# Kernel tuning notes

Hardware: AMD Instinct MI355X
Metric: run time of the kernel (lower is better)

Reference implementation:

```python
import jax, jax.numpy as jnp
import numpy as np

B, S, D, H = 2, 2048, 1024, 16
DK = D // H


def setup_inputs() -> dict:
    key = jax.random.key(0)
    ks = jax.random.split(key, 12)
    scale = 1.0 / np.sqrt(D)
    inp = {
        "Q": jax.random.normal(ks[0], (B, S, D), jnp.float32),
        "K": jax.random.normal(ks[1], (B, S, D), jnp.float32),
        "V": jax.random.normal(ks[2], (B, S, D), jnp.float32),
        # causal mask, broadcastable to [B, H, S, S]; 0 -> masked
        "Mask": jnp.tril(jnp.ones((S, S), jnp.int32))[None, None],
        "Wq": jax.random.normal(ks[3], (D, D), jnp.float32) * scale,
        "bq": jnp.zeros((D,), jnp.float32),
        "Wk": jax.random.normal(ks[4], (D, D), jnp.float32) * scale,
        "bk": jnp.zeros((D,), jnp.float32),
        "Wv": jax.random.normal(ks[5], (D, D), jnp.float32) * scale,
        "bv": jnp.zeros((D,), jnp.float32),
        "Wo": jax.random.normal(ks[6], (D, D), jnp.float32) * scale,
        "bo": jnp.zeros((D,), jnp.float32),
    }
    return inp


def _heads(x):
    # [B, S, D] -> [B, H, S, DK]
    return x.reshape(B, S, H, DK).transpose(0, 2, 1, 3)


def reference(Q, K, V, Mask, Wq, bq, Wk, bk, Wv, bv, Wo, bo):
    q = _heads(Q @ Wq.T + bq)
    k = _heads(K @ Wk.T + bk)
    v = _heads(V @ Wv.T + bv)
    # NOTE: original module does NOT scale by 1/sqrt(d_k)
    logits = jnp.einsum("bhqd,bhkd->bhqk", q, k)
    logits = jnp.where(Mask == 0, jnp.float32(-1e9), logits)
    attn = jax.nn.softmax(logits, axis=-1)  # dropout p=0.0 -> identity
    ctx = jnp.einsum("bhqk,bhkd->bhqd", attn, v)
    ctx = ctx.transpose(0, 2, 1, 3).reshape(B, S, D)
    return ctx @ Wo.T + bo
```

## Files before the change

### kernel.cpp

```cpp
#include <hip/hip_runtime.h>
#include <hip/hip_bf16.h>

#define B_  2
#define S_  2048
#define D_  1024
#define H_  16
#define DK_ 64
#define M_  (B_ * S_)

typedef __bf16 bf16;
typedef __bf16 bf16x8 __attribute__((ext_vector_type(8)));
typedef __bf16 bf16x4 __attribute__((ext_vector_type(4)));
typedef float  f32x4  __attribute__((ext_vector_type(4)));

#define MFMA16(a, b, c) __builtin_amdgcn_mfma_f32_16x16x32_bf16((a), (b), (c), 0, 0, 0)

__device__ __forceinline__ void gl2lds16(const bf16* g, bf16* l) {
    __builtin_amdgcn_global_load_lds((const __attribute__((address_space(1))) void*)g,
                                     (__attribute__((address_space(3))) void*)l, 16, 0, 0);
}

struct CastArgs { const float* src[7]; bf16* dst[7]; };

__global__ __launch_bounds__(256) void cast_all(CastArgs a) {
    int i = blockIdx.x * 256 + threadIdx.x;
    int seg, off;
    if (i < 3145728) { seg = i >> 20; off = i & 1048575; }
    else { int j = i - 3145728; seg = 3 + (j >> 18); off = j & 262143; }
    float4 v = ((const float4*)a.src[seg])[off];
    bf16x4 o;
    o[0] = (bf16)v.x; o[1] = (bf16)v.y; o[2] = (bf16)v.z; o[3] = (bf16)v.w;
    *(bf16x4*)&a.dst[seg][(size_t)off * 4] = o;
}

struct QkvArgs { const bf16* A[3]; const bf16* W[3]; const float* bias[3]; bf16* out[3]; };

__global__ __launch_bounds__(256, 3) void gemm_qkv(QkvArgs ar) {
    __shared__ char smem[34816];
    bf16* As = (bf16*)smem;
    bf16* Bs = (bf16*)(smem + 16384);
    bf16* Cs = (bf16*)smem;

    const int hid = (blockIdx.z * gridDim.y + blockIdx.y) * gridDim.x + blockIdx.x;
    const int swz = (hid & 7) * 96 + (hid >> 3);
    const int bx = swz & 7, by = (swz >> 3) & 31, z = swz >> 8;

    const bf16* A  = ar.A[z];
    const bf16* Bt = ar.W[z];
    const float* bias = ar.bias[z];
    bf16* Out = ar.out[z];
    const int mode = (z == 2) ? 1 : 0;

    const int t = threadIdx.x, lane = t & 63, w = t >> 6;
    const int lr = lane & 15, lq = lane >> 4;
    const int wm = (w >> 1) * 64, wn = (w & 1) * 64;
    const int n0 = bx * 128, m0 = by * 128;

    const bf16* Ag[4]; const bf16* Bg[4]; bf16* Al[4]; bf16* Bl[4];
#pragma unroll
    for (int i = 0; i < 4; ++i) {
        int c = i * 256 + w * 64 + lane;
        int row = c >> 3, x = (c & 7) ^ (row & 7);
        Ag[i] = A  + (size_t)(m0 + row) * 1024 + x * 8;
        Bg[i] = Bt + (size_t)(n0 + row) * 1024 + x * 8;
        Al[i] = As + (i * 256 + w * 64) * 8;
        Bl[i] = Bs + (i * 256 + w * 64) * 8;
    }

    f32x4 acc[4][4];
#pragma unroll
    for (int mi = 0; mi < 4; ++mi)
#pragma unroll
        for (int ni = 0; ni < 4; ++ni) acc[mi][ni] = 0.0f;

    for (int k0 = 0; k0 < 1024; k0 += 64) {
        __syncthreads();
#pragma unroll
        for (int i = 0; i < 4; ++i) {
            gl2lds16(Ag[i] + k0, Al[i]);
            gl2lds16(Bg[i] + k0, Bl[i]);
        }
        __syncthreads();
#pragma unroll
        for (int ks = 0; ks < 2; ++ks) {
            bf16x8 af[4], bfr[4];
#pragma unroll
            for (int mi = 0; mi < 4; ++mi) {
                int row = wm + mi * 16 + lr;
                af[mi] = *(const bf16x8*)&As[row * 64 + ((ks * 4 + lq) ^ (row & 7)) * 8];
            }
#pragma unroll
            for (int ni = 0; ni < 4; ++ni) {
                int row = wn + ni * 16 + lr;
                bfr[ni] = *(const bf16x8*)&Bs[row * 64 + ((ks * 4 + lq) ^ (row & 7)) * 8];
            }
#pragma unroll
            for (int mi = 0; mi < 4; ++mi)
#pragma unroll
                for (int ni = 0; ni < 4; ++ni) acc[mi][ni] = MFMA16(af[mi], bfr[ni], acc[mi][ni]);
        }
    }

    if (mode == 0) {
#pragma unroll
        for (int mi = 0; mi < 4; ++mi) {
#pragma unroll
            for (int ni = 0; ni < 4; ++ni) {
                int gn = n0 + wn + ni * 16 + lr;
                float bv = bias[gn];
#pragma unroll
                for (int r = 0; r < 4; ++r) {
                    int gm = m0 + wm + mi * 16 + lq * 4 + r;
                    float v = acc[mi][ni][r] + bv;
                    int b = gm >> 11, s = gm & (S_ - 1);
                    int h = gn >> 6, dk = gn & 63;
                    Out[(((size_t)(b * H_ + h) * S_ + s) << 6) + dk] = (bf16)v;
                }
            }
        }
    } else {
        __syncthreads();
#pragma unroll
        for (int mi = 0; mi < 4; ++mi) {
#pragma unroll
            for (int ni = 0; ni < 4; ++ni) {
                int n = wn + ni * 16 + lr;
                float bv = bias[n0 + n];
                bf16x4 pk;
#pragma unroll
                for (int r = 0; r < 4; ++r) pk[r] = (bf16)(acc[mi][ni][r] + bv);
                *(bf16x4*)&Cs[n * 136 + wm + mi * 16 + lq * 4] = pk;
            }
        }
        __syncthreads();
        const int b = m0 >> 11, s0 = m0 & (S_ - 1);
#pragma unroll
        for (int j = 0; j < 8; ++j) {
            int cc = j * 256 + t;
            int n = cc >> 4, cm = cc & 15;
            int gn = n0 + n, h = gn >> 6, dk = gn & 63;
            bf16x8 v = *(const bf16x8*)&Cs[n * 136 + cm * 8];
            *(bf16x8*)&Out[(((size_t)(b * H_ + h) * DK_ + dk) << 11) + s0 + cm * 8] = v;
        }
    }
}

__global__ __launch_bounds__(256, 2) void gemm_out(const bf16* __restrict__ A,
                                                   const bf16* __restrict__ Bt,
                                                   const float* __restrict__ bias,
                                                   float* __restrict__ Out) {
    __shared__ bf16 As[64 * 64];
    __shared__ bf16 Bs[128 * 64];

    const int hid = blockIdx.y * gridDim.x + blockIdx.x;
    const int swz = (hid & 7) * 64 + (hid >> 3);
    const int bx = swz & 7, by = swz >> 3;

    const int t = threadIdx.x, lane = t & 63, w = t >> 6;
    const int lr = lane & 15, lq = lane >> 4;
    const int wm = (w >> 1) * 32, wn = (w & 1) * 64;
    const int n0 = bx * 128, m0 = by * 64;

    const bf16* Ag[2]; bf16* Al[2];
#pragma unroll
    for (int i = 0; i < 2; ++i) {
        int c = i * 256 + w * 64 + lane;
        int row = c >> 3, x = (c & 7) ^ (row & 7);
        Ag[i] = A + (size_t)(m0 + row) * 1024 + x * 8;
        Al[i] = As + (i * 256 + w * 64) * 8;
    }
    const bf16* Bg[4]; bf16* Bl[4];
#pragma unroll
    for (int i = 0; i < 4; ++i) {
        int c = i * 256 + w * 64 + lane;
        int row = c >> 3, x = (c & 7) ^ (row & 7);
        Bg[i] = Bt + (size_t)(n0 + row) * 1024 + x * 8;
        Bl[i] = Bs + (i * 256 + w * 64) * 8;
    }

    f32x4 acc[2][4];
#pragma unroll
    for (int mi = 0; mi < 2; ++mi)
#pragma unroll
        for (int ni = 0; ni < 4; ++ni) acc[mi][ni] = 0.0f;

    for (int k0 = 0; k0 < 1024; k0 += 64) {
        __syncthreads();
#pragma unroll
        for (int i = 0; i < 2; ++i) gl2lds16(Ag[i] + k0, Al[i]);
#pragma unroll
        for (int i = 0; i < 4; ++i) gl2lds16(Bg[i] + k0, Bl[i]);
        __syncthreads();
#pragma unroll
        for (int ks = 0; ks < 2; ++ks) {
            bf16x8 af[2], bfr[4];
#pragma unroll
            for (int mi = 0; mi < 2; ++mi) {
                int row = wm + mi * 16 + lr;
                af[mi] = *(const bf16x8*)&As[row * 64 + ((ks * 4 + lq) ^ (row & 7)) * 8];
            }
#pragma unroll
            for (int ni = 0; ni < 4; ++ni) {
                int row = wn + ni * 16 + lr;
                bfr[ni] = *(const bf16x8*)&Bs[row * 64 + ((ks * 4 + lq) ^ (row & 7)) * 8];
            }
#pragma unroll
            for (int mi = 0; mi < 2; ++mi)
#pragma unroll
                for (int ni = 0; ni < 4; ++ni) acc[mi][ni] = MFMA16(af[mi], bfr[ni], acc[mi][ni]);
        }
    }

#pragma unroll
    for (int mi = 0; mi < 2; ++mi) {
#pragma unroll
        for (int ni = 0; ni < 4; ++ni) {
            int gn = n0 + wn + ni * 16 + lr;
            float bv = bias[gn];
#pragma unroll
            for (int r = 0; r < 4; ++r) {
                int gm = m0 + wm + mi * 16 + lq * 4 + r;
                Out[(size_t)gm * 1024 + gn] = acc[mi][ni][r] + bv;
            }
        }
    }
}

__global__ __launch_bounds__(256, 2) void flash_attn(const bf16* __restrict__ qh,
                                                     const bf16* __restrict__ kh,
                                                     const bf16* __restrict__ vt,
                                                     bf16* __restrict__ ctx) {
    __shared__ char smem[33280];
    bf16* Ks = (bf16*)smem;
    bf16* Ps = (bf16*)(smem + 16384);
    float* Op = (float*)(smem + 16384);
    float* Lh = (float*)(smem + 32768);

    const int id = blockIdx.x;
    const int xcd = id & 7, loc = id >> 3;
    const int bh = xcd * 4 + (loc & 3);
    const int pair = loc >> 2;
    const int b = bh >> 4, h = bh & 15;

    const bf16* Qp = qh + (size_t)bh * S_ * DK_;
    const bf16* Kp = kh + (size_t)bh * S_ * DK_;
    const bf16* Vp = vt + (size_t)bh * DK_ * S_;

    const int t = threadIdx.x, lane = t & 63, w = t >> 6;
    const int lr = lane & 15, lq = lane >> 4;
    const int wq = w & 1, wk = w >> 1;
    bf16* Pw = Ps + w * 2048;

    for (int half = 0; half < 2; ++half) {
        const int qt = half ? (31 - pair) : pair;

        bf16x8 qreg[2][2];
#pragma unroll
        for (int ks = 0; ks < 2; ++ks)
#pragma unroll
            for (int nt = 0; nt < 2; ++nt)
                qreg[ks][nt] = *(const bf16x8*)(Qp +
                    (size_t)(qt * 64 + wq * 32 + nt * 16 + lr) * 64 + ks * 32 + lq * 8);

        f32x4 oacc[2][4];
#pragma unroll
        for (int mt = 0; mt < 2; ++mt)
#pragma unroll
            for (int nt = 0; nt < 4; ++nt) oacc[mt][nt] = 0.0f;
        float lpart[2] = {0.f, 0.f};

        const int nkt = qt / 2 + 1;
        for (int kt = 0; kt < nkt; ++kt) {
            __syncthreads();
#pragma unroll
            for (int i = 0; i < 4; ++i) {
                int c = w * 256 + i * 64 + lane;
                int krow = c >> 3, xx = (c & 7) ^ (krow & 7);
                gl2lds16(Kp + (size_t)(kt * 128 + krow) * 64 + xx * 8, Ks + (w * 256 + i * 64) * 8);
            }
            __syncthreads();

            const int k64 = kt * 2 + wk;
            if (k64 <= qt) {
                bf16x8 bv[2][4];
#pragma unroll
                for (int kk = 0; kk < 2; ++kk)
#pragma unroll
                    for (int nt = 0; nt < 4; ++nt)
                        bv[kk][nt] = *(const bf16x8*)(Vp + (size_t)(nt * 16 + lr) * S_ +
                                                      kt * 128 + wk * 64 + kk * 32 + lq * 8);
                f32x4 s[4][2];
#pragma unroll
                for (int mt = 0; mt < 4; ++mt)
#pragma unroll
                    for (int nt = 0; nt < 2; ++nt) s[mt][nt] = 0.0f;
                __builtin_amdgcn_s_setprio(1);
#pragma unroll
                for (int ks = 0; ks < 2; ++ks) {
                    bf16x8 af[4];
                    int xx = (ks * 4 + lq) ^ (lr & 7);
#pragma unroll
                    for (int mt = 0; mt < 4; ++mt)
                        af[mt] = *(const bf16x8*)&Ks[(wk * 64 + mt * 16 + lr) * 64 + xx * 8];
#pragma unroll
                    for (int mt = 0; mt < 4; ++mt)
#pragma unroll
                        for (int nt = 0; nt < 2; ++nt) s[mt][nt] = MFMA16(af[mt], qreg[ks][nt], s[mt][nt]);
                }
                __builtin_amdgcn_s_setprio(0);
                const bool diag = (k64 == qt);
#pragma unroll
                for (int mt = 0; mt < 4; ++mt)
#pragma unroll
                    for (int nt = 0; nt < 2; ++nt) {
                        bf16x4 pb;
#pragma unroll
                        for (int r = 0; r < 4; ++r) {
                            int kl = mt * 16 + lq * 4 + r;
                            int qlT = wq * 32 + nt * 16 + lr;
                            float p = (!diag || kl <= qlT) ? __expf(s[mt][nt][r]) : 0.0f;
                            bf16 p16 = (bf16)p;
                            lpart[nt] += (float)p16;
                            pb[r] = p16;
                        }
                        int xx = (2 * mt + (lq >> 1)) ^ (lr & 7);
                        *(bf16x4*)&Pw[(nt * 16 + lr) * 64 + xx * 8 + (lq & 1) * 4] = pb;
                    }
                __builtin_amdgcn_s_setprio(1);
#pragma unroll
                for (int kk = 0; kk < 2; ++kk) {
                    bf16x8 ap[2];
                    int xx = (kk * 4 + lq) ^ (lr & 7);
#pragma unroll
                    for (int mt2 = 0; mt2 < 2; ++mt2)
                        ap[mt2] = *(const bf16x8*)&Pw[(mt2 * 16 + lr) * 64 + xx * 8];
#pragma unroll
                    for (int mt2 = 0; mt2 < 2; ++mt2)
#pragma unroll
                        for (int nt = 0; nt < 4; ++nt)
                            oacc[mt2][nt] = MFMA16(ap[mt2], bv[kk][nt], oacc[mt2][nt]);
                }
                __builtin_amdgcn_s_setprio(0);
            }
        }

        __syncthreads();
#pragma unroll
        for (int nt = 0; nt < 2; ++nt) {
            lpart[nt] += __shfl_xor(lpart[nt], 16);
            lpart[nt] += __shfl_xor(lpart[nt], 32);
        }
        if (lq == 0)
#pragma unroll
            for (int nt = 0; nt < 2; ++nt) Lh[wk * 64 + wq * 32 + nt * 16 + lr] = lpart[nt];
        if (wk == 1) {
#pragma unroll
            for (int mt = 0; mt < 2; ++mt)
#pragma unroll
                for (int nt = 0; nt < 4; ++nt)
#pragma unroll
                    for (int r = 0; r < 4; ++r) {
                        int row = mt * 16 + lq * 4 + r, col = nt * 16 + lr;
                        int xx = (col >> 2) ^ (row & 15);
                        Op[wq * 2048 + row * 64 + xx * 4 + (col & 3)] = oacc[mt][nt][r];
                    }
        }
        __syncthreads();
        if (wk == 0) {
            float linv[2][4];
#pragma unroll
            for (int mt = 0; mt < 2; ++mt)
#pragma unroll
                for (int r = 0; r < 4; ++r) {
                    int qq = wq * 32 + mt * 16 + lq * 4 + r;
                    linv[mt][r] = 1.0f / (Lh[qq] + Lh[64 + qq]);
                }
#pragma unroll
            for (int mt = 0; mt < 2; ++mt)
#pragma unroll
                for (int nt = 0; nt < 4; ++nt)
#pragma unroll
                    for (int r = 0; r < 4; ++r) {
                        int row = mt * 16 + lq * 4 + r, col = nt * 16 + lr;
                        int xx = (col >> 2) ^ (row & 15);
                        float v = (oacc[mt][nt][r] + Op[wq * 2048 + row * 64 + xx * 4 + (col & 3)]) * linv[mt][r];
                        int q = qt * 64 + wq * 32 + row;
                        ctx[((size_t)(b * S_ + q)) * D_ + h * DK_ + col] = (bf16)v;
                    }
        }
        __syncthreads();
    }
}

extern "C" void kernel_launch(void* const* d_in, const int* in_sizes, int n_in,
                              void* d_out, int out_size, void* d_ws, size_t ws_size,
                              hipStream_t stream) {
    const float* Q  = (const float*)d_in[0];
    const float* K  = (const float*)d_in[1];
    const float* V  = (const float*)d_in[2];
    const float* Wq = (const float*)d_in[4];
    const float* bq = (const float*)d_in[5];
    const float* Wk = (const float*)d_in[6];
    const float* bk = (const float*)d_in[7];
    const float* Wv = (const float*)d_in[8];
    const float* bv = (const float*)d_in[9];
    const float* Wo = (const float*)d_in[10];
    const float* bo = (const float*)d_in[11];

    char* p = (char*)d_ws;
    bf16* Qb  = (bf16*)p;  p += (size_t)M_ * D_ * 2;
    bf16* Kb  = (bf16*)p;  p += (size_t)M_ * D_ * 2;
    bf16* Vb  = (bf16*)p;  p += (size_t)M_ * D_ * 2;
    bf16* Wqb = (bf16*)p;  p += (size_t)D_ * D_ * 2;
    bf16* Wkb = (bf16*)p;  p += (size_t)D_ * D_ * 2;
    bf16* Wvb = (bf16*)p;  p += (size_t)D_ * D_ * 2;
    bf16* Wob = (bf16*)p;  p += (size_t)D_ * D_ * 2;
    bf16* qhd = (bf16*)p;  p += (size_t)M_ * D_ * 2;
    bf16* khd = (bf16*)p;  p += (size_t)M_ * D_ * 2;
    bf16* vtr = (bf16*)p;  p += (size_t)M_ * D_ * 2;
    bf16* ctx = (bf16*)p;  p += (size_t)M_ * D_ * 2;

    CastArgs ca;
    ca.src[0] = Q;  ca.dst[0] = Qb;
    ca.src[1] = K;  ca.dst[1] = Kb;
    ca.src[2] = V;  ca.dst[2] = Vb;
    ca.src[3] = Wq; ca.dst[3] = Wqb;
    ca.src[4] = Wk; ca.dst[4] = Wkb;
    ca.src[5] = Wv; ca.dst[5] = Wvb;
    ca.src[6] = Wo; ca.dst[6] = Wob;
    cast_all<<<16384, 256, 0, stream>>>(ca);

    QkvArgs qa;
    qa.A[0] = Qb;  qa.A[1] = Kb;  qa.A[2] = Vb;
    qa.W[0] = Wqb; qa.W[1] = Wkb; qa.W[2] = Wvb;
    qa.bias[0] = bq; qa.bias[1] = bk; qa.bias[2] = bv;
    qa.out[0] = qhd; qa.out[1] = khd; qa.out[2] = vtr;
    dim3 qgrid(D_ / 128, M_ / 128, 3);
    gemm_qkv<<<qgrid, 256, 0, stream>>>(qa);

    flash_attn<<<512, 256, 0, stream>>>(qhd, khd, vtr, ctx);

    dim3 ogrid(D_ / 128, M_ / 64);
    gemm_out<<<ogrid, 256, 0, stream>>>(ctx, Wob, bo, (float*)d_out);
}
```

Baseline: 223.5 us.

## Process both paired query tiles in one K loop sharing K tile loads

The attention kernel previously handled its two query tiles (pair and 31-pair) in sequence, loading K tiles into LDS separately for each. Now both tiles' Q fragments and accumulators stay live in registers, and a single K loop over the longer tile's range serves both, running the short tile only while its causal bound allows. This removes the duplicated K global-to-LDS loads and barriers for the overlapping range. The cost is roughly double the accumulator and Q register footprint, which can lower occupancy or cause spills.

```diff
diff --git a/kernel.cpp b/kernel.cpp
--- a/kernel.cpp
+++ b/kernel.cpp
@@ -251,99 +251,107 @@
     const int wq = w & 1, wk = w >> 1;
     bf16* Pw = Ps + w * 2048;
 
-    for (int half = 0; half < 2; ++half) {
-        const int qt = half ? (31 - pair) : pair;
-
-        bf16x8 qreg[2][2];
-#pragma unroll
-        for (int ks = 0; ks < 2; ++ks)
-#pragma unroll
-            for (int nt = 0; nt < 2; ++nt)
-                qreg[ks][nt] = *(const bf16x8*)(Qp +
-                    (size_t)(qt * 64 + wq * 32 + nt * 16 + lr) * 64 + ks * 32 + lq * 8);
-
-        f32x4 oacc[2][4];
-#pragma unroll
-        for (int mt = 0; mt < 2; ++mt)
-#pragma unroll
-            for (int nt = 0; nt < 4; ++nt) oacc[mt][nt] = 0.0f;
-        float lpart[2] = {0.f, 0.f};
-
-        const int nkt = qt / 2 + 1;
-        for (int kt = 0; kt < nkt; ++kt) {
-            __syncthreads();
-#pragma unroll
-            for (int i = 0; i < 4; ++i) {
-                int c = w * 256 + i * 64 + lane;
-                int krow = c >> 3, xx = (c & 7) ^ (krow & 7);
-                gl2lds16(Kp + (size_t)(kt * 128 + krow) * 64 + xx * 8, Ks + (w * 256 + i * 64) * 8);
-            }
-            __syncthreads();
-
-            const int k64 = kt * 2 + wk;
-            if (k64 <= qt) {
-                bf16x8 bv[2][4];
-#pragma unroll
-                for (int kk = 0; kk < 2; ++kk)
-#pragma unroll
-                    for (int nt = 0; nt < 4; ++nt)
-                        bv[kk][nt] = *(const bf16x8*)(Vp + (size_t)(nt * 16 + lr) * S_ +
-                                                      kt * 128 + wk * 64 + kk * 32 + lq * 8);
-                f32x4 s[4][2];
-#pragma unroll
-                for (int mt = 0; mt < 4; ++mt)
-#pragma unroll
-                    for (int nt = 0; nt < 2; ++nt) s[mt][nt] = 0.0f;
-                __builtin_amdgcn_s_setprio(1);
-#pragma unroll
-                for (int ks = 0; ks < 2; ++ks) {
-                    bf16x8 af[4];
-                    int xx = (ks * 4 + lq) ^ (lr & 7);
-#pragma unroll
-                    for (int mt = 0; mt < 4; ++mt)
-                        af[mt] = *(const bf16x8*)&Ks[(wk * 64 + mt * 16 + lr) * 64 + xx * 8];
-#pragma unroll
-                    for (int mt = 0; mt < 4; ++mt)
-#pragma unroll
-                        for (int nt = 0; nt < 2; ++nt) s[mt][nt] = MFMA16(af[mt], qreg[ks][nt], s[mt][nt]);
+    const int qtA = pair;
+    const int qtB = 31 - pair;
+    const int nktB = qtB / 2 + 1;
+
+    bf16x8 qregA[2][2], qregB[2][2];
+#pragma unroll
+    for (int ks = 0; ks < 2; ++ks)
+#pragma unroll
+        for (int nt = 0; nt < 2; ++nt) {
+            qregA[ks][nt] = *(const bf16x8*)(Qp +
+                (size_t)(qtA * 64 + wq * 32 + nt * 16 + lr) * 64 + ks * 32 + lq * 8);
+            qregB[ks][nt] = *(const bf16x8*)(Qp +
+                (size_t)(qtB * 64 + wq * 32 + nt * 16 + lr) * 64 + ks * 32 + lq * 8);
+        }
+
+    f32x4 oaccA[2][4], oaccB[2][4];
+#pragma unroll
+    for (int mt = 0; mt < 2; ++mt)
+#pragma unroll
+        for (int nt = 0; nt < 4; ++nt) { oaccA[mt][nt] = 0.0f; oaccB[mt][nt] = 0.0f; }
+    float lpartA[2] = {0.f, 0.f}, lpartB[2] = {0.f, 0.f};
+
+    auto body = [&](f32x4 (&oacc)[2][4], float (&lpart)[2],
+                    const bf16x8 (&qreg)[2][2], int qt, int kt, int k64) {
+        bf16x8 bv[2][4];
+#pragma unroll
+        for (int kk = 0; kk < 2; ++kk)
+#pragma unroll
+            for (int nt = 0; nt < 4; ++nt)
+                bv[kk][nt] = *(const bf16x8*)(Vp + (size_t)(nt * 16 + lr) * S_ +
+                                              kt * 128 + wk * 64 + kk * 32 + lq * 8);
+        f32x4 s[4][2];
+#pragma unroll
+        for (int mt = 0; mt < 4; ++mt)
+#pragma unroll
+            for (int nt = 0; nt < 2; ++nt) s[mt][nt] = 0.0f;
+        __builtin_amdgcn_s_setprio(1);
+#pragma unroll
+        for (int ks = 0; ks < 2; ++ks) {
+            bf16x8 af[4];
+            int xx = (ks * 4 + lq) ^ (lr & 7);
+#pragma unroll
+            for (int mt = 0; mt < 4; ++mt)
+                af[mt] = *(const bf16x8*)&Ks[(wk * 64 + mt * 16 + lr) * 64 + xx * 8];
+#pragma unroll
+            for (int mt = 0; mt < 4; ++mt)
+#pragma unroll
+                for (int nt = 0; nt < 2; ++nt) s[mt][nt] = MFMA16(af[mt], qreg[ks][nt], s[mt][nt]);
+        }
+        __builtin_amdgcn_s_setprio(0);
+        const bool diag = (k64 == qt);
+#pragma unroll
+        for (int mt = 0; mt < 4; ++mt)
+#pragma unroll
+            for (int nt = 0; nt < 2; ++nt) {
+                bf16x4 pb;
+#pragma unroll
+                for (int r = 0; r < 4; ++r) {
+                    int kl = mt * 16 + lq * 4 + r;
+                    int qlT = wq * 32 + nt * 16 + lr;
+                    float p = (!diag || kl <= qlT) ? __expf(s[mt][nt][r]) : 0.0f;
+                    bf16 p16 = (bf16)p;
+                    lpart[nt] += (float)p16;
+                    pb[r] = p16;
                 }
-                __builtin_amdgcn_s_setprio(0);
-                const bool diag = (k64 == qt);
-#pragma unroll
-                for (int mt = 0; mt < 4; ++mt)
-#pragma unroll
-                    for (int nt = 0; nt < 2; ++nt) {
-                        bf16x4 pb;
-#pragma unroll
-                        for (int r = 0; r < 4; ++r) {
-                            int kl = mt * 16 + lq * 4 + r;
-                            int qlT = wq * 32 + nt * 16 + lr;
-                            float p = (!diag || kl <= qlT) ? __expf(s[mt][nt][r]) : 0.0f;
-                            bf16 p16 = (bf16)p;
-                            lpart[nt] += (float)p16;
-                            pb[r] = p16;
-                        }
-                        int xx = (2 * mt + (lq >> 1)) ^ (lr & 7);
-                        *(bf16x4*)&Pw[(nt * 16 + lr) * 64 + xx * 8 + (lq & 1) * 4] = pb;
-                    }
-                __builtin_amdgcn_s_setprio(1);
-#pragma unroll
-                for (int kk = 0; kk < 2; ++kk) {
-                    bf16x8 ap[2];
-                    int xx = (kk * 4 + lq) ^ (lr & 7);
-#pragma unroll
-                    for (int mt2 = 0; mt2 < 2; ++mt2)
-                        ap[mt2] = *(const bf16x8*)&Pw[(mt2 * 16 + lr) * 64 + xx * 8];
-#pragma unroll
-                    for (int mt2 = 0; mt2 < 2; ++mt2)
-#pragma unroll
-                        for (int nt = 0; nt < 4; ++nt)
-                            oacc[mt2][nt] = MFMA16(ap[mt2], bv[kk][nt], oacc[mt2][nt]);
-                }
-                __builtin_amdgcn_s_setprio(0);
-            }
-        }
-
+                int xx = (2 * mt + (lq >> 1)) ^ (lr & 7);
+                *(bf16x4*)&Pw[(nt * 16 + lr) * 64 + xx * 8 + (lq & 1) * 4] = pb;
+            }
+        __builtin_amdgcn_s_setprio(1);
+#pragma unroll
+        for (int kk = 0; kk < 2; ++kk) {
+            bf16x8 ap[2];
+            int xx = (kk * 4 + lq) ^ (lr & 7);
+#pragma unroll
+            for (int mt2 = 0; mt2 < 2; ++mt2)
+                ap[mt2] = *(const bf16x8*)&Pw[(mt2 * 16 + lr) * 64 + xx * 8];
+#pragma unroll
+            for (int mt2 = 0; mt2 < 2; ++mt2)
+#pragma unroll
+                for (int nt = 0; nt < 4; ++nt)
+                    oacc[mt2][nt] = MFMA16(ap[mt2], bv[kk][nt], oacc[mt2][nt]);
+        }
+        __builtin_amdgcn_s_setprio(0);
+    };
+
+    for (int kt = 0; kt < nktB; ++kt) {
+        __syncthreads();
+#pragma unroll
+        for (int i = 0; i < 4; ++i) {
+            int c = w * 256 + i * 64 + lane;
+            int krow = c >> 3, xx = (c & 7) ^ (krow & 7);
+            gl2lds16(Kp + (size_t)(kt * 128 + krow) * 64 + xx * 8, Ks + (w * 256 + i * 64) * 8);
+        }
+        __syncthreads();
+
+        const int k64 = kt * 2 + wk;
+        if (k64 <= qtB) body(oaccB, lpartB, qregB, qtB, kt, k64);
+        if (k64 <= qtA) body(oaccA, lpartA, qregA, qtA, kt, k64);
+    }
+
+    auto epi = [&](f32x4 (&oacc)[2][4], float (&lpart)[2], int qt) {
         __syncthreads();
 #pragma unroll
         for (int nt = 0; nt < 2; ++nt) {
@@ -388,8 +396,10 @@
                         ctx[((size_t)(b * S_ + q)) * D_ + h * DK_ + col] = (bf16)v;
                     }
         }
-        __syncthreads();
-    }
+    };
+    epi(oaccA, lpartA, qtA);
+    __syncthreads();
+    epi(oaccB, lpartB, qtB);
 }
 
 extern "C" void kernel_launch(void* const* d_in, const int* in_sizes, int n_in,
```

Result: faster. 217.1 us (-2.8%).
